# Optimization experiments

Hardware: AMD Instinct MI355X
Metric: run time of the kernel (lower is better)

Reference implementation:

```python
import jax, jax.numpy as jnp
import numpy as np

H = 32          # total heads
K = 8           # active heads per token
D = 128         # head_dim = embed_dim // active_heads
E = 1024        # embed_dim
S = 1024        # seq_len
MAX_SEQ = 8192
BASE = 10000.0
SCALE = D ** -0.5
LB_W = 0.01
ENT_W = 0.01


def _rope(v, cos, sin):
    # v: (T, D); cos/sin: (T, D)
    v1, v2 = v[:, : D // 2], v[:, D // 2:]
    rot = jnp.concatenate([-v2, v1], axis=-1)
    return v * cos + rot * sin


def setup_inputs() -> dict:
    key = jax.random.key(0)
    ks = jax.random.split(key, 6)
    x = jax.random.normal(ks[0], (1, S, E), jnp.float32)
    Wq = jax.random.normal(ks[1], (E, H * D), jnp.float32) * 0.02
    Wk = jax.random.normal(ks[2], (E, H * D), jnp.float32) * 0.02
    Wv = jax.random.normal(ks[3], (E, H * D), jnp.float32) * 0.02
    Wr = jax.random.normal(ks[4], (E, H), jnp.float32) * 0.02
    Wo = jax.random.normal(ks[5], (K * D, E), jnp.float32) * 0.02
    head_counts = jnp.zeros((1, H), jnp.int32)
    return {"x": x, "Wq": Wq, "Wk": Wk, "Wv": Wv, "Wr": Wr, "Wo": Wo,
            "head_counts": head_counts}


def reference(x, Wq, Wk, Wv, Wr, Wo, head_counts):
    # ---- routing (eval mode: no gumbel noise) ----
    logits = x @ Wr                                   # (1, S, H)
    soft_probs = jax.nn.softmax(logits, axis=-1)
    top_logits, head_idx = jax.lax.top_k(logits, K)   # (1, S, K)
    head_w = jax.nn.softmax(top_logits, axis=-1)      # (1, S, K)

    # ---- aux loss ----
    primary = head_idx[..., 0]                        # (1, S)
    one_hot_p = jax.nn.one_hot(primary, H, dtype=jnp.float32)
    f = one_hot_p.mean(axis=1)                        # (1, H)
    p = soft_probs.mean(axis=1)                       # (1, H)
    balance = H * (f * p).sum(axis=-1).mean()
    entropy = -(soft_probs * jnp.log(soft_probs + 1e-8)).sum(axis=-1)
    entropy_loss = -entropy.mean()
    z_loss = (jax.nn.logsumexp(logits, axis=-1) ** 2).mean() * 0.01
    aux_loss = LB_W * balance + ENT_W * entropy_loss + z_loss

    # ---- projections + per-token gather of selected heads ----
    q_all = (x @ Wq).reshape(1, S, H, D)
    k_all = (x @ Wk).reshape(1, S, H, D)
    v_all = (x @ Wv).reshape(1, S, H, D)
    gidx = head_idx[..., None]                        # (1, S, K, 1)
    q = jnp.take_along_axis(q_all, gidx, axis=2)[0].reshape(S * K, D)
    k = jnp.take_along_axis(k_all, gidx, axis=2)[0].reshape(S * K, D)
    v = jnp.take_along_axis(v_all, gidx, axis=2)[0].reshape(S * K, D)

    heads_flat = head_idx[0].reshape(S * K)           # (T,)

    # rank of each dispatched token within its head (exclusive prefix count)
    oh = jax.nn.one_hot(heads_flat, H, dtype=jnp.int32)   # (T, H)
    excl = jnp.cumsum(oh, axis=0) - oh
    rank = jnp.take_along_axis(excl, heads_flat[:, None], axis=1)[:, 0]
    positions = rank + head_counts[0, heads_flat]
    positions = jnp.clip(positions, 0, MAX_SEQ - 1)

    # ---- per-head RoPE with per-head position counters ----
    inv_freq = 1.0 / (BASE ** (jnp.arange(0, D, 2, dtype=jnp.float32) / D))
    freqs = positions.astype(jnp.float32)[:, None] * inv_freq[None, :]
    emb = jnp.concatenate([freqs, freqs], axis=-1)    # (T, D)
    cos, sin = jnp.cos(emb), jnp.sin(emb)
    q = _rope(q, cos, sin)
    k = _rope(k, cos, sin)

    # ---- block-diagonal-causal attention (same head, earlier dispatch order) ----
    idx = jnp.arange(S * K)
    mask = (heads_flat[:, None] == heads_flat[None, :]) & (idx[None, :] <= idx[:, None])
    scores = (q @ k.T) * SCALE                        # (T, T)
    scores = jnp.where(mask, scores, jnp.float32(-1e30))
    attn = jax.nn.softmax(scores, axis=-1)
    out = attn @ v                                    # (T, D)

    # ---- combine with routing weights + output projection ----
    out = out.reshape(S, K, D) * head_w[0][..., None]
    out = out.reshape(S, K * D) @ Wo                  # (S, E)
    output = out[None]                                # (1, S, E)

    updated_counts = head_counts + oh.sum(axis=0)[None]
    return output, updated_counts, aux_loss
```

## Files before the change

kernel.cpp:

```cpp
#include <hip/hip_runtime.h>
#include <math.h>

#define S 1024
#define E 1024
#define H 32
#define KSEL 8
#define D 128
#define HD 4096
#define SK 8192
#define MAXL 1024
#define CAP 9216
#define ATTN_SCALE 0.08838834764831845f
#define SSTR 36
#define PSTR 40

typedef _Float16 half8 __attribute__((ext_vector_type(8)));
typedef _Float16 half4 __attribute__((ext_vector_type(4)));
typedef float floatx4 __attribute__((ext_vector_type(4)));
typedef float floatx16 __attribute__((ext_vector_type(16)));
typedef float f4 __attribute__((ext_vector_type(4)));

#define GLOAD_LDS16(gsrc, ldst) \
    __builtin_amdgcn_global_load_lds( \
        (const __attribute__((address_space(1))) void*)(gsrc), \
        (__attribute__((address_space(3))) void*)(ldst), 16, 0, 0)

__global__ __launch_bounds__(256) void router_kernel(
    const float* __restrict__ x, const float* __restrict__ Wr,
    int* __restrict__ head_idx, float* __restrict__ head_w,
    float* __restrict__ pbuf, float* __restrict__ entz,
    _Float16* __restrict__ xh)
{
    int tid = threadIdx.x;
    int s = blockIdx.x * 4 + (tid >> 6);
    int lane = tid & 63;
    int h = lane & 31, half = lane >> 5;
    const float* xr = x + (size_t)s * E + half * 512;
    const float* wr = Wr + (size_t)(half * 512) * H + h;
    float acc = 0.f;
    #pragma unroll 8
    for (int e = 0; e < 512; ++e)
        acc += xr[e] * wr[e * H];
    acc += __shfl_xor(acc, 32, 64);
    float logit = acc;
    float m = logit;
    #pragma unroll
    for (int off = 16; off; off >>= 1) m = fmaxf(m, __shfl_xor(m, off, 64));
    float ex = expf(logit - m);
    float Z = ex;
    #pragma unroll
    for (int off = 16; off; off >>= 1) Z += __shfl_xor(Z, off, 64);
    float p = ex / Z;
    float es = p * logf(p + 1e-8f);
    #pragma unroll
    for (int off = 16; off; off >>= 1) es += __shfl_xor(es, off, 64);
    float lse = m + logf(Z);
    float lv = logit;
    float tv[KSEL]; int ti[KSEL];
    #pragma unroll
    for (int j = 0; j < KSEL; ++j) {
        float bv = lv; int bi = h;
        #pragma unroll
        for (int off = 16; off; off >>= 1) {
            float ov = __shfl_xor(bv, off, 64);
            int oi = __shfl_xor(bi, off, 64);
            if (ov > bv || (ov == bv && oi < bi)) { bv = ov; bi = oi; }
        }
        tv[j] = bv; ti[j] = bi;
        if (h == bi) lv = -INFINITY;
    }
    float Z2 = 0.f;
    #pragma unroll
    for (int j = 0; j < KSEL; ++j) Z2 += expf(tv[j] - tv[0]);
    if (lane < 32) pbuf[s * 32 + lane] = p;
    if (lane == 0) {
        entz[s * 2]     = es;
        entz[s * 2 + 1] = lse * lse;
        #pragma unroll
        for (int j = 0; j < KSEL; ++j) {
            head_idx[s * KSEL + j] = ti[j];
            head_w[s * KSEL + j]   = expf(tv[j] - tv[0]) / Z2;
        }
    }
    const float* xrow = x + (size_t)s * E;
    _Float16* xhrow = xh + (size_t)s * E;
    #pragma unroll
    for (int t = 0; t < 4; ++t) {
        int e = t * 256 + lane * 4;
        f4 v = *(const f4*)&xrow[e];
        half4 o;
        o.x = (_Float16)v.x; o.y = (_Float16)v.y; o.z = (_Float16)v.z; o.w = (_Float16)v.w;
        *(half4*)&xhrow[e] = o;
    }
}

__global__ __launch_bounds__(256) void aux_kernel(
    const float* __restrict__ pbuf, const float* __restrict__ entz,
    const int* __restrict__ head_idx, float* __restrict__ out_aux)
{
    int tid = threadIdx.x;
    int h = tid & 31, grp = tid >> 5;
    __shared__ float red[256], red2[256];
    __shared__ float psum[32];
    __shared__ int hist[32];
    if (tid < 32) hist[tid] = 0;
    float ps = 0.f;
    for (int s = grp; s < S; s += 8) ps += pbuf[s * 32 + h];
    red[tid] = ps;
    float es = 0.f, zs = 0.f;
    for (int s = tid; s < S; s += 256) { es += entz[s * 2]; zs += entz[s * 2 + 1]; }
    red2[tid] = es;
    __syncthreads();
    if (grp == 0) {
        float v = 0.f;
        #pragma unroll
        for (int j = 0; j < 8; ++j) v += red[j * 32 + h];
        psum[h] = v;
    }
    __syncthreads();
    red[tid] = zs;
    for (int s = tid; s < S; s += 256)
        atomicAdd(&hist[head_idx[s * KSEL]], 1);
    __syncthreads();
    for (int stp = 128; stp; stp >>= 1) {
        if (tid < stp) { red[tid] += red[tid + stp]; red2[tid] += red2[tid + stp]; }
        __syncthreads();
    }
    if (tid == 0) {
        float bal = 0.f;
        for (int hh = 0; hh < H; ++hh)
            bal += ((float)hist[hh] / (float)S) * (psum[hh] / (float)S);
        bal *= (float)H;
        float ent_loss = red2[0] / (float)S;
        float z = red[0] / (float)S * 0.01f;
        out_aux[0] = 0.01f * bal + 0.01f * ent_loss + z;
    }
}

__global__ __launch_bounds__(256) void order_kernel(
    const int* __restrict__ head_idx, const int* __restrict__ head_counts,
    int* __restrict__ order, int* __restrict__ hlen, float* __restrict__ out_counts)
{
    int h = blockIdx.x, tid = threadIdx.x;
    int wave = tid >> 6, lane = tid & 63;
    __shared__ int wtot[4];
    int base = 0;
    int hc = head_counts[h];
    int v = head_idx[tid];
    for (int c0 = 0; c0 < SK; c0 += 256) {
        int vn = (c0 + 256 < SK) ? head_idx[c0 + 256 + tid] : 0;
        bool pred = (v == h);
        unsigned long long mask = __ballot(pred);
        int within = __popcll(mask & ((1ull << lane) - 1ull));
        if (lane == 0) wtot[wave] = __popcll(mask);
        __syncthreads();
        int pre = 0, tot = 0;
        #pragma unroll
        for (int w = 0; w < 4; ++w) { int t = wtot[w]; if (w < wave) pre += t; tot += t; }
        if (pred) order[h * MAXL + base + pre + within] = c0 + tid;
        base += tot;
        __syncthreads();
        v = vn;
    }
    if (tid == 0) {
        hlen[h] = base;
        out_counts[h] = (float)(hc + base);
    }
}

__global__ void offs_kernel(const int* __restrict__ hlen, int* __restrict__ hstart)
{
    if (threadIdx.x == 0 && blockIdx.x == 0) {
        int acc = 0;
        for (int h = 0; h < H; ++h) {
            hstart[h] = acc;
            acc += (hlen[h] + 31) & ~31;
        }
    }
}

__global__ __launch_bounds__(256) void convW_kernel(
    const float* __restrict__ Wq, const float* __restrict__ Wk,
    const float* __restrict__ Wv, const float* __restrict__ Wo,
    _Float16* __restrict__ Wqkt, _Float16* __restrict__ Wot)
{
    int z = blockIdx.z;
    if (z == 3 && blockIdx.y >= 16) return;
    const float* W = (z == 0) ? Wq : (z == 1) ? Wk : (z == 2) ? Wv : Wo;
    _Float16* T = (z < 3) ? (Wqkt + (size_t)z * HD * E) : Wot;
    int C = (z < 3) ? HD : 1024;
    int r0 = blockIdx.x * 64, c0 = blockIdx.y * 64;
    int t = threadIdx.x;
    __shared__ float tile[64][65];
    #pragma unroll
    for (int p = 0; p < 4; ++p) {
        int idx = p * 256 + t;
        int r = idx >> 4, cq = (idx & 15) * 4;
        f4 v = *(const f4*)&W[(size_t)(r0 + r) * C + c0 + cq];
        tile[r][cq] = v.x; tile[r][cq + 1] = v.y; tile[r][cq + 2] = v.z; tile[r][cq + 3] = v.w;
    }
    __syncthreads();
    #pragma unroll
    for (int p = 0; p < 4; ++p) {
        int idx = p * 256 + t;
        int c = idx >> 4, rq = (idx & 15) * 4;
        half4 o;
        o.x = (_Float16)tile[rq][c];
        o.y = (_Float16)tile[rq + 1][c];
        o.z = (_Float16)tile[rq + 2][c];
        o.w = (_Float16)tile[rq + 3][c];
        *(half4*)&T[(size_t)(c0 + c) * 1024 + r0 + rq] = o;
    }
}

__global__ __launch_bounds__(256) void qkv_mfma(
    const _Float16* __restrict__ xh, const _Float16* __restrict__ Wt,
    const int* __restrict__ order, const int* __restrict__ hlen,
    const int* __restrict__ hstart, const int* __restrict__ head_counts,
    _Float16* __restrict__ qh, _Float16* __restrict__ kh, _Float16* __restrict__ vT)
{
    int xid = blockIdx.x;
    int qkv = xid >> 5, h = xid & 31;
    int rt = blockIdx.y;
    int len = hlen[h];
    int row0 = rt * 64;
    if (row0 >= len) return;
    int hb = hstart[h];
    int lenp = (len + 31) & ~31;
    int tid = threadIdx.x, wave = tid >> 6, lane = tid & 63;
    int wm = wave >> 1, wn = wave & 1;
    int l32 = lane & 31, g = lane >> 5;

    __shared__ _Float16 As[2][64 * 64];
    __shared__ _Float16 Bs[2][128 * 64];
    __shared__ int stok[64];

    if (tid < 64) {
        int r = row0 + tid;
        stok[tid] = (r < len) ? (order[h * MAXL + r] >> 3) : 0;
    }
    __syncthreads();

    const _Float16* Wb = Wt + (size_t)((qkv * H + h) * D) * E;

    auto stage = [&](int buf, int k0) {
        #pragma unroll
        for (int it = 0; it < 2; ++it) {
            int f = it * 256 + tid;
            int row = f >> 3, c = f & 7;
            int sc = c ^ (row & 7);
            const _Float16* src = xh + (size_t)stok[row] * E + k0 + sc * 8;
            GLOAD_LDS16(src, &As[buf][f * 8]);
        }
        #pragma unroll
        for (int it = 0; it < 4; ++it) {
            int f = it * 256 + tid;
            int row = f >> 3, c = f & 7;
            int sc = c ^ (row & 7);
            const _Float16* src = Wb + (size_t)row * E + k0 + sc * 8;
            GLOAD_LDS16(src, &Bs[buf][f * 8]);
        }
    };

    floatx16 acc[2] = {};
    int arow = wm * 32 + l32;

    auto compute = [&](int buf) {
        #pragma unroll
        for (int ks = 0; ks < 4; ++ks) {
            int wchunk = ks * 2 + g;
            half8 af = *(const half8*)&As[buf][arow * 64 + (wchunk ^ (arow & 7)) * 8];
            #pragma unroll
            for (int nf = 0; nf < 2; ++nf) {
                int brow = wn * 64 + nf * 32 + l32;
                half8 bf = *(const half8*)&Bs[buf][brow * 64 + (wchunk ^ (brow & 7)) * 8];
                acc[nf] = __builtin_amdgcn_mfma_f32_32x32x16_f16(af, bf, acc[nf], 0, 0, 0);
            }
        }
    };

    stage(0, 0);
    __syncthreads();
    int buf = 0;
    for (int k0 = 64; k0 < E; k0 += 64) {
        stage(buf ^ 1, k0);
        compute(buf);
        __syncthreads();
        buf ^= 1;
    }
    compute(buf);

    if (qkv < 2) {
        _Float16* dst = (qkv == 0) ? qh : kh;
        float* scr = (float*)&Bs[0][0];
        __syncthreads();
        #pragma unroll
        for (int nf = 0; nf < 2; ++nf) {
            int col = wn * 64 + nf * 32 + l32;
            #pragma unroll
            for (int reg = 0; reg < 16; ++reg) {
                int rl = wm * 32 + (reg & 3) + 8 * (reg >> 2) + 4 * g;
                scr[rl * 128 + col] = acc[nf][reg];
            }
        }
        __syncthreads();
        int hc = head_counts[h];
        #pragma unroll
        for (int pass = 0; pass < 16; ++pass) {
            int idx = pass * 256 + tid;
            int r = idx >> 6, d2 = idx & 63;
            int slot = row0 + r;
            if (slot < len) {
                float v1 = scr[r * 128 + d2], v2 = scr[r * 128 + 64 + d2];
                int p = slot + hc;
                p = p < 0 ? 0 : (p > 8191 ? 8191 : p);
                float inv = exp2f((float)d2 * -0.20762050f);
                float ang = (float)p * inv;
                float cs = cosf(ang), sn = sinf(ang);
                _Float16* dp = dst + ((size_t)hb + slot) * D;
                dp[d2]      = (_Float16)(v1 * cs - v2 * sn);
                dp[d2 + 64] = (_Float16)(v2 * cs + v1 * sn);
            }
        }
    } else {
        #pragma unroll
        for (int nf = 0; nf < 2; ++nf) {
            int col = wn * 64 + nf * 32 + l32;
            #pragma unroll
            for (int q4 = 0; q4 < 4; ++q4) {
                int slot0 = row0 + wm * 32 + 8 * q4 + 4 * g;
                _Float16* vp = vT + (size_t)hb * D + (size_t)col * lenp + slot0;
                if (slot0 + 3 < len) {
                    half4 o;
                    o.x = (_Float16)acc[nf][q4 * 4 + 0];
                    o.y = (_Float16)acc[nf][q4 * 4 + 1];
                    o.z = (_Float16)acc[nf][q4 * 4 + 2];
                    o.w = (_Float16)acc[nf][q4 * 4 + 3];
                    *(half4*)vp = o;
                } else {
                    #pragma unroll
                    for (int r2 = 0; r2 < 4; ++r2)
                        if (slot0 + r2 < len) vp[r2] = (_Float16)acc[nf][q4 * 4 + r2];
                }
            }
        }
    }
}

__global__ __launch_bounds__(64) void attn_mfma(
    const _Float16* __restrict__ qh, const _Float16* __restrict__ kh,
    const _Float16* __restrict__ vT,
    const int* __restrict__ order, const int* __restrict__ hlen,
    const int* __restrict__ hstart, const float* __restrict__ head_w,
    _Float16* __restrict__ ao)
{
    int h = blockIdx.x >> 5, qt = blockIdx.x & 31;
    int len = hlen[h];
    int row0 = qt * 32;
    if (row0 >= len) return;
    int hb = hstart[h];
    int lenp = (len + 31) & ~31;
    int lane = threadIdx.x;
    int l32 = lane & 31, g = lane >> 5;
    int srow = lane >> 1, shalf = lane & 1;

    __shared__ float Sld[32 * SSTR];
    __shared__ _Float16 Pld[32 * PSTR];
    __shared__ float alphaLd[32];
    __shared__ float scLd[32];
    __shared__ int flatLd[32];

    if (lane < 32) {
        int r = row0 + lane;
        flatLd[lane] = (r < len) ? order[h * MAXL + r] : -1;
    }

    const _Float16* qrow = qh + ((size_t)hb + row0 + l32) * D;
    half8 qf[8];
    #pragma unroll
    for (int t = 0; t < 8; ++t) qf[t] = *(const half8*)(qrow + t * 16 + g * 8);

    floatx16 O[4] = {};
    float m_run = -INFINITY, l_run = 0.f;
    __syncthreads();

    half8 kf[8], kfn[8], vv[8];
    {
        const _Float16* krow = kh + ((size_t)hb + l32) * D;
        #pragma unroll
        for (int t = 0; t < 8; ++t) kf[t] = *(const half8*)(krow + t * 16 + g * 8);
    }

    for (int kt = 0; kt <= qt; ++kt) {
        int col0 = kt * 32;
        floatx16 Sc = {};
        #pragma unroll
        for (int t = 0; t < 8; ++t)
            Sc = __builtin_amdgcn_mfma_f32_32x32x16_f16(qf[t], kf[t], Sc, 0, 0, 0);
        #pragma unroll
        for (int nt = 0; nt < 4; ++nt) {
            const _Float16* vp = vT + (size_t)hb * D + (size_t)(nt * 32 + l32) * lenp + col0;
            vv[nt * 2]     = *(const half8*)(vp + g * 8);
            vv[nt * 2 + 1] = *(const half8*)(vp + 16 + g * 8);
        }
        if (kt < qt) {
            const _Float16* krow = kh + ((size_t)hb + col0 + 32 + l32) * D;
            #pragma unroll
            for (int t = 0; t < 8; ++t) kfn[t] = *(const half8*)(krow + t * 16 + g * 8);
        }
        bool diag = (kt == qt);
        #pragma unroll
        for (int reg = 0; reg < 16; ++reg) {
            int row = (reg & 3) + 8 * (reg >> 2) + 4 * g;
            float s = Sc[reg] * ATTN_SCALE;
            if (diag && l32 > row) s = -1e30f;
            Sld[row * SSTR + l32] = s;
        }
        __syncthreads();
        const float* sp = &Sld[srow * SSTR + shalf * 16];
        float va[16];
        *(f4*)(va)      = *(const f4*)(sp);
        *(f4*)(va + 4)  = *(const f4*)(sp + 4);
        *(f4*)(va + 8)  = *(const f4*)(sp + 8);
        *(f4*)(va + 12) = *(const f4*)(sp + 12);
        float mt_ = va[0];
        #pragma unroll
        for (int j = 1; j < 16; ++j) mt_ = fmaxf(mt_, va[j]);
        mt_ = fmaxf(mt_, __shfl_xor(mt_, 1, 64));
        float m_new = fmaxf(m_run, mt_);
        float alpha = __expf(m_run - m_new);
        float p[16], tsum = 0.f;
        #pragma unroll
        for (int j = 0; j < 16; ++j) { p[j] = __expf(va[j] - m_new); tsum += p[j]; }
        tsum += __shfl_xor(tsum, 1, 64);
        l_run = l_run * alpha + tsum;
        m_run = m_new;
        half8 ph0, ph1;
        #pragma unroll
        for (int j = 0; j < 8; ++j) { ph0[j] = (_Float16)p[j]; ph1[j] = (_Float16)p[j + 8]; }
        *(half8*)&Pld[srow * PSTR + shalf * 16]     = ph0;
        *(half8*)&Pld[srow * PSTR + shalf * 16 + 8] = ph1;
        if (shalf == 0) alphaLd[srow] = alpha;
        __syncthreads();
        f4 al[4];
        #pragma unroll
        for (int qq = 0; qq < 4; ++qq) al[qq] = *(const f4*)&alphaLd[4 * g + 8 * qq];
        #pragma unroll
        for (int reg = 0; reg < 16; ++reg) {
            float av = al[reg >> 2][reg & 3];
            O[0][reg] *= av; O[1][reg] *= av; O[2][reg] *= av; O[3][reg] *= av;
        }
        half8 pf0 = *(const half8*)&Pld[l32 * PSTR + g * 8];
        half8 pf1 = *(const half8*)&Pld[l32 * PSTR + 16 + g * 8];
        #pragma unroll
        for (int nt = 0; nt < 4; ++nt) {
            O[nt] = __builtin_amdgcn_mfma_f32_32x32x16_f16(pf0, vv[nt * 2],     O[nt], 0, 0, 0);
            O[nt] = __builtin_amdgcn_mfma_f32_32x32x16_f16(pf1, vv[nt * 2 + 1], O[nt], 0, 0, 0);
        }
        __syncthreads();
        #pragma unroll
        for (int t = 0; t < 8; ++t) kf[t] = kfn[t];
    }
    if (shalf == 0) {
        int flat = flatLd[srow];
        float hw = (flat >= 0) ? head_w[flat] : 0.f;
        scLd[srow] = hw / l_run;
    }
    __syncthreads();
    float scr[16]; int flr[16];
    #pragma unroll
    for (int reg = 0; reg < 16; ++reg) {
        int row = (reg & 3) + 8 * (reg >> 2) + 4 * g;
        scr[reg] = scLd[row];
        flr[reg] = flatLd[row];
    }
    #pragma unroll
    for (int nt = 0; nt < 4; ++nt) {
        int col = nt * 32 + l32;
        #pragma unroll
        for (int reg = 0; reg < 16; ++reg) {
            if (flr[reg] >= 0)
                ao[(size_t)flr[reg] * D + col] = (_Float16)(O[nt][reg] * scr[reg]);
        }
    }
}

__global__ __launch_bounds__(256) void out_mfma(
    const _Float16* __restrict__ A, const _Float16* __restrict__ Bt,
    float* __restrict__ C)
{
    int n0 = blockIdx.x * 64, m0 = blockIdx.y * 64;
    int tid = threadIdx.x, wave = tid >> 6, lane = tid & 63;
    int wm = wave >> 1, wn = wave & 1;
    int l32 = lane & 31, g = lane >> 5;

    __shared__ _Float16 As[2][64 * 64];
    __shared__ _Float16 Bs[2][64 * 64];

    auto stage = [&](int buf, int k0) {
        #pragma unroll
        for (int it = 0; it < 2; ++it) {
            int f = it * 256 + tid;
            int row = f >> 3, c = f & 7;
            int sc = c ^ (row & 7);
            GLOAD_LDS16(A + (size_t)(m0 + row) * 1024 + k0 + sc * 8, &As[buf][f * 8]);
        }
        #pragma unroll
        for (int it = 0; it < 2; ++it) {
            int f = it * 256 + tid;
            int row = f >> 3, c = f & 7;
            int sc = c ^ (row & 7);
            GLOAD_LDS16(Bt + (size_t)(n0 + row) * 1024 + k0 + sc * 8, &Bs[buf][f * 8]);
        }
    };

    floatx16 acc = {};
    int arow = wm * 32 + l32;
    int brow = wn * 32 + l32;

    auto compute = [&](int buf) {
        #pragma unroll
        for (int ks = 0; ks < 4; ++ks) {
            int wchunk = ks * 2 + g;
            half8 af = *(const half8*)&As[buf][arow * 64 + (wchunk ^ (arow & 7)) * 8];
            half8 bf = *(const half8*)&Bs[buf][brow * 64 + (wchunk ^ (brow & 7)) * 8];
            acc = __builtin_amdgcn_mfma_f32_32x32x16_f16(af, bf, acc, 0, 0, 0);
        }
    };

    stage(0, 0);
    __syncthreads();
    int buf = 0;
    for (int k0 = 64; k0 < 1024; k0 += 64) {
        stage(buf ^ 1, k0);
        compute(buf);
        __syncthreads();
        buf ^= 1;
    }
    compute(buf);

    int col = n0 + wn * 32 + l32;
    #pragma unroll
    for (int reg = 0; reg < 16; ++reg) {
        int row = m0 + wm * 32 + (reg & 3) + 8 * (reg >> 2) + 4 * g;
        C[(size_t)row * 1024 + col] = acc[reg];
    }
}

extern "C" void kernel_launch(void* const* d_in, const int* in_sizes, int n_in,
                              void* d_out, int out_size, void* d_ws, size_t ws_size,
                              hipStream_t stream)
{
    const float* x  = (const float*)d_in[0];
    const float* Wq = (const float*)d_in[1];
    const float* Wk = (const float*)d_in[2];
    const float* Wv = (const float*)d_in[3];
    const float* Wr = (const float*)d_in[4];
    const float* Wo = (const float*)d_in[5];
    const int* head_counts = (const int*)d_in[6];
    float* out = (float*)d_out;

    float* head_w = (float*)d_ws;
    float* pbuf   = head_w + SK;
    float* entz   = pbuf + S * 32;
    int* head_idx = (int*)(entz + S * 2);
    int* order    = head_idx + SK;
    int* hlen     = order + H * MAXL;
    int* hstart   = hlen + 32;
    _Float16* xh   = (_Float16*)(hstart + 32);
    _Float16* aoh  = xh + (size_t)S * E;
    _Float16* Wqkt = aoh + (size_t)SK * D;
    _Float16* Wot  = Wqkt + (size_t)3 * HD * E;
    _Float16* qh   = Wot + (size_t)1024 * 1024;
    _Float16* kh   = qh + (size_t)CAP * D;
    _Float16* vT   = kh + (size_t)CAP * D;

    convW_kernel<<<dim3(16, 64, 4), 256, 0, stream>>>(Wq, Wk, Wv, Wo, Wqkt, Wot);
    router_kernel<<<S / 4, 256, 0, stream>>>(x, Wr, head_idx, head_w, pbuf, entz, xh);
    order_kernel<<<H, 256, 0, stream>>>(head_idx, head_counts, order, hlen,
                                        out + (size_t)S * E);
    offs_kernel<<<1, 64, 0, stream>>>(hlen, hstart);
    qkv_mfma<<<dim3(96, 16), 256, 0, stream>>>(xh, Wqkt, order, hlen, hstart, head_counts,
                                               qh, kh, vT);
    attn_mfma<<<H * 32, 64, 0, stream>>>(qh, kh, vT, order, hlen, hstart, head_w, aoh);
    out_mfma<<<dim3(16, 16), 256, 0, stream>>>(aoh, Wot, out);
    aux_kernel<<<1, 256, 0, stream>>>(pbuf, entz, head_idx, out + (size_t)S * E + H);
}
```

Before: 239.2 us.

## Split attention KV loop across two waves, fold aux and offsets kernels away

Attention blocks now use two waves that each handle alternating key tiles, then merge their partial softmax states (max and sum) through shared memory before the scaled output is written. This shortens the serial per-block loop for long causal rows. The aux-loss kernel is merged into order_kernel as an extra block, and the offset kernel is replaced by recomputing the per-head prefix sum inside qkv and attention. The router dot product also uses four accumulators. Together these remove two launches and add shared-memory use and a merge step in attention.

```diff
diff --git a/kernel.cpp b/kernel.cpp
--- a/kernel.cpp
+++ b/kernel.cpp
@@ -37,10 +37,15 @@
     int h = lane & 31, half = lane >> 5;
     const float* xr = x + (size_t)s * E + half * 512;
     const float* wr = Wr + (size_t)(half * 512) * H + h;
-    float acc = 0.f;
-    #pragma unroll 8
-    for (int e = 0; e < 512; ++e)
-        acc += xr[e] * wr[e * H];
+    float a0 = 0.f, a1 = 0.f, a2 = 0.f, a3 = 0.f;
+    #pragma unroll 4
+    for (int e = 0; e < 512; e += 4) {
+        a0 += xr[e]     * wr[e * H];
+        a1 += xr[e + 1] * wr[(e + 1) * H];
+        a2 += xr[e + 2] * wr[(e + 2) * H];
+        a3 += xr[e + 3] * wr[(e + 3) * H];
+    }
+    float acc = (a0 + a1) + (a2 + a3);
     acc += __shfl_xor(acc, 32, 64);
     float logit = acc;
     float m = logit;
@@ -94,54 +99,52 @@
     }
 }
 
-__global__ __launch_bounds__(256) void aux_kernel(
-    const float* __restrict__ pbuf, const float* __restrict__ entz,
-    const int* __restrict__ head_idx, float* __restrict__ out_aux)
-{
-    int tid = threadIdx.x;
-    int h = tid & 31, grp = tid >> 5;
-    __shared__ float red[256], red2[256];
-    __shared__ float psum[32];
-    __shared__ int hist[32];
-    if (tid < 32) hist[tid] = 0;
-    float ps = 0.f;
-    for (int s = grp; s < S; s += 8) ps += pbuf[s * 32 + h];
-    red[tid] = ps;
-    float es = 0.f, zs = 0.f;
-    for (int s = tid; s < S; s += 256) { es += entz[s * 2]; zs += entz[s * 2 + 1]; }
-    red2[tid] = es;
-    __syncthreads();
-    if (grp == 0) {
-        float v = 0.f;
-        #pragma unroll
-        for (int j = 0; j < 8; ++j) v += red[j * 32 + h];
-        psum[h] = v;
-    }
-    __syncthreads();
-    red[tid] = zs;
-    for (int s = tid; s < S; s += 256)
-        atomicAdd(&hist[head_idx[s * KSEL]], 1);
-    __syncthreads();
-    for (int stp = 128; stp; stp >>= 1) {
-        if (tid < stp) { red[tid] += red[tid + stp]; red2[tid] += red2[tid + stp]; }
-        __syncthreads();
-    }
-    if (tid == 0) {
-        float bal = 0.f;
-        for (int hh = 0; hh < H; ++hh)
-            bal += ((float)hist[hh] / (float)S) * (psum[hh] / (float)S);
-        bal *= (float)H;
-        float ent_loss = red2[0] / (float)S;
-        float z = red[0] / (float)S * 0.01f;
-        out_aux[0] = 0.01f * bal + 0.01f * ent_loss + z;
-    }
-}
-
 __global__ __launch_bounds__(256) void order_kernel(
     const int* __restrict__ head_idx, const int* __restrict__ head_counts,
-    int* __restrict__ order, int* __restrict__ hlen, float* __restrict__ out_counts)
+    int* __restrict__ order, int* __restrict__ hlen, float* __restrict__ out_counts,
+    const float* __restrict__ pbuf, const float* __restrict__ entz,
+    float* __restrict__ out_aux)
 {
     int h = blockIdx.x, tid = threadIdx.x;
+    if (h == H) {
+        int hh = tid & 31, grp = tid >> 5;
+        __shared__ float red[256], red2[256];
+        __shared__ float psum[32];
+        __shared__ int hist[32];
+        if (tid < 32) hist[tid] = 0;
+        float ps = 0.f;
+        for (int s = grp; s < S; s += 8) ps += pbuf[s * 32 + hh];
+        red[tid] = ps;
+        float es = 0.f, zs = 0.f;
+        for (int s = tid; s < S; s += 256) { es += entz[s * 2]; zs += entz[s * 2 + 1]; }
+        red2[tid] = es;
+        __syncthreads();
+        if (grp == 0) {
+            float v = 0.f;
+            #pragma unroll
+            for (int j = 0; j < 8; ++j) v += red[j * 32 + hh];
+            psum[hh] = v;
+        }
+        __syncthreads();
+        red[tid] = zs;
+        for (int s = tid; s < S; s += 256)
+            atomicAdd(&hist[head_idx[s * KSEL]], 1);
+        __syncthreads();
+        for (int stp = 128; stp; stp >>= 1) {
+            if (tid < stp) { red[tid] += red[tid + stp]; red2[tid] += red2[tid + stp]; }
+            __syncthreads();
+        }
+        if (tid == 0) {
+            float bal = 0.f;
+            for (int j = 0; j < H; ++j)
+                bal += ((float)hist[j] / (float)S) * (psum[j] / (float)S);
+            bal *= (float)H;
+            float ent_loss = red2[0] / (float)S;
+            float z = red[0] / (float)S * 0.01f;
+            out_aux[0] = 0.01f * bal + 0.01f * ent_loss + z;
+        }
+        return;
+    }
     int wave = tid >> 6, lane = tid & 63;
     __shared__ int wtot[4];
     int base = 0;
@@ -165,17 +168,6 @@
     if (tid == 0) {
         hlen[h] = base;
         out_counts[h] = (float)(hc + base);
-    }
-}
-
-__global__ void offs_kernel(const int* __restrict__ hlen, int* __restrict__ hstart)
-{
-    if (threadIdx.x == 0 && blockIdx.x == 0) {
-        int acc = 0;
-        for (int h = 0; h < H; ++h) {
-            hstart[h] = acc;
-            acc += (hlen[h] + 31) & ~31;
-        }
     }
 }
 
@@ -216,7 +208,7 @@
 __global__ __launch_bounds__(256) void qkv_mfma(
     const _Float16* __restrict__ xh, const _Float16* __restrict__ Wt,
     const int* __restrict__ order, const int* __restrict__ hlen,
-    const int* __restrict__ hstart, const int* __restrict__ head_counts,
+    const int* __restrict__ head_counts,
     _Float16* __restrict__ qh, _Float16* __restrict__ kh, _Float16* __restrict__ vT)
 {
     int xid = blockIdx.x;
@@ -225,7 +217,8 @@
     int len = hlen[h];
     int row0 = rt * 64;
     if (row0 >= len) return;
-    int hb = hstart[h];
+    int hb = 0;
+    for (int i = 0; i < h; ++i) hb += (hlen[i] + 31) & ~31;
     int lenp = (len + 31) & ~31;
     int tid = threadIdx.x, wave = tid >> 6, lane = tid & 63;
     int wm = wave >> 1, wn = wave & 1;
@@ -347,32 +340,35 @@
     }
 }
 
-__global__ __launch_bounds__(64) void attn_mfma(
+__global__ __launch_bounds__(128) void attn_mfma(
     const _Float16* __restrict__ qh, const _Float16* __restrict__ kh,
     const _Float16* __restrict__ vT,
     const int* __restrict__ order, const int* __restrict__ hlen,
-    const int* __restrict__ hstart, const float* __restrict__ head_w,
-    _Float16* __restrict__ ao)
+    const float* __restrict__ head_w, _Float16* __restrict__ ao)
 {
     int h = blockIdx.x >> 5, qt = blockIdx.x & 31;
     int len = hlen[h];
     int row0 = qt * 32;
     if (row0 >= len) return;
-    int hb = hstart[h];
+    int hb = 0;
+    for (int i = 0; i < h; ++i) hb += (hlen[i] + 31) & ~31;
     int lenp = (len + 31) & ~31;
-    int lane = threadIdx.x;
+    int tid = threadIdx.x;
+    int w = tid >> 6, lane = tid & 63;
     int l32 = lane & 31, g = lane >> 5;
     int srow = lane >> 1, shalf = lane & 1;
 
-    __shared__ float Sld[32 * SSTR];
-    __shared__ _Float16 Pld[32 * PSTR];
-    __shared__ float alphaLd[32];
-    __shared__ float scLd[32];
+    __shared__ float Sld[2][32 * SSTR];
+    __shared__ _Float16 Pld[2][32 * PSTR];
+    __shared__ float alphaLd[2][32];
+    __shared__ float mlLd[32][4];
+    __shared__ float facLd[32][3];
     __shared__ int flatLd[32];
-
-    if (lane < 32) {
-        int r = row0 + lane;
-        flatLd[lane] = (r < len) ? order[h * MAXL + r] : -1;
+    __shared__ float Obuf[32][128];
+
+    if (tid < 32) {
+        int r = row0 + tid;
+        flatLd[tid] = (r < len) ? order[h * MAXL + r] : -1;
     }
 
     const _Float16* qrow = qh + ((size_t)hb + row0 + l32) * D;
@@ -382,105 +378,125 @@
 
     floatx16 O[4] = {};
     float m_run = -INFINITY, l_run = 0.f;
+
+    if (w <= qt) {
+        half8 kf[8], kfn[8], vv[8];
+        {
+            const _Float16* krow = kh + ((size_t)hb + w * 32 + l32) * D;
+            #pragma unroll
+            for (int t = 0; t < 8; ++t) kf[t] = *(const half8*)(krow + t * 16 + g * 8);
+        }
+        for (int kt = w; kt <= qt; kt += 2) {
+            int col0 = kt * 32;
+            floatx16 Sc = {};
+            #pragma unroll
+            for (int t = 0; t < 8; ++t)
+                Sc = __builtin_amdgcn_mfma_f32_32x32x16_f16(qf[t], kf[t], Sc, 0, 0, 0);
+            #pragma unroll
+            for (int nt = 0; nt < 4; ++nt) {
+                const _Float16* vp = vT + (size_t)hb * D + (size_t)(nt * 32 + l32) * lenp + col0;
+                vv[nt * 2]     = *(const half8*)(vp + g * 8);
+                vv[nt * 2 + 1] = *(const half8*)(vp + 16 + g * 8);
+            }
+            if (kt + 2 <= qt) {
+                const _Float16* krow = kh + ((size_t)hb + col0 + 64 + l32) * D;
+                #pragma unroll
+                for (int t = 0; t < 8; ++t) kfn[t] = *(const half8*)(krow + t * 16 + g * 8);
+            }
+            bool diag = (kt == qt);
+            #pragma unroll
+            for (int reg = 0; reg < 16; ++reg) {
+                int row = (reg & 3) + 8 * (reg >> 2) + 4 * g;
+                float s = Sc[reg] * ATTN_SCALE;
+                if (diag && l32 > row) s = -1e30f;
+                Sld[w][row * SSTR + l32] = s;
+            }
+            __builtin_amdgcn_wave_barrier();
+            const float* sp = &Sld[w][srow * SSTR + shalf * 16];
+            float va[16];
+            *(f4*)(va)      = *(const f4*)(sp);
+            *(f4*)(va + 4)  = *(const f4*)(sp + 4);
+            *(f4*)(va + 8)  = *(const f4*)(sp + 8);
+            *(f4*)(va + 12) = *(const f4*)(sp + 12);
+            float mt_ = va[0];
+            #pragma unroll
+            for (int j = 1; j < 16; ++j) mt_ = fmaxf(mt_, va[j]);
+            mt_ = fmaxf(mt_, __shfl_xor(mt_, 1, 64));
+            float m_new = fmaxf(m_run, mt_);
+            float alpha = __expf(m_run - m_new);
+            float p[16], tsum = 0.f;
+            #pragma unroll
+            for (int j = 0; j < 16; ++j) { p[j] = __expf(va[j] - m_new); tsum += p[j]; }
+            tsum += __shfl_xor(tsum, 1, 64);
+            l_run = l_run * alpha + tsum;
+            m_run = m_new;
+            half8 ph0, ph1;
+            #pragma unroll
+            for (int j = 0; j < 8; ++j) { ph0[j] = (_Float16)p[j]; ph1[j] = (_Float16)p[j + 8]; }
+            *(half8*)&Pld[w][srow * PSTR + shalf * 16]     = ph0;
+            *(half8*)&Pld[w][srow * PSTR + shalf * 16 + 8] = ph1;
+            if (shalf == 0) alphaLd[w][srow] = alpha;
+            __builtin_amdgcn_wave_barrier();
+            f4 al[4];
+            #pragma unroll
+            for (int qq = 0; qq < 4; ++qq) al[qq] = *(const f4*)&alphaLd[w][4 * g + 8 * qq];
+            #pragma unroll
+            for (int reg = 0; reg < 16; ++reg) {
+                float av = al[reg >> 2][reg & 3];
+                O[0][reg] *= av; O[1][reg] *= av; O[2][reg] *= av; O[3][reg] *= av;
+            }
+            half8 pf0 = *(const half8*)&Pld[w][l32 * PSTR + g * 8];
+            half8 pf1 = *(const half8*)&Pld[w][l32 * PSTR + 16 + g * 8];
+            #pragma unroll
+            for (int nt = 0; nt < 4; ++nt) {
+                O[nt] = __builtin_amdgcn_mfma_f32_32x32x16_f16(pf0, vv[nt * 2],     O[nt], 0, 0, 0);
+                O[nt] = __builtin_amdgcn_mfma_f32_32x32x16_f16(pf1, vv[nt * 2 + 1], O[nt], 0, 0, 0);
+            }
+            __builtin_amdgcn_wave_barrier();
+            #pragma unroll
+            for (int t = 0; t < 8; ++t) kf[t] = kfn[t];
+        }
+    }
+    if (shalf == 0) { mlLd[srow][w * 2] = m_run; mlLd[srow][w * 2 + 1] = l_run; }
     __syncthreads();
-
-    half8 kf[8], kfn[8], vv[8];
-    {
-        const _Float16* krow = kh + ((size_t)hb + l32) * D;
-        #pragma unroll
-        for (int t = 0; t < 8; ++t) kf[t] = *(const half8*)(krow + t * 16 + g * 8);
-    }
-
-    for (int kt = 0; kt <= qt; ++kt) {
-        int col0 = kt * 32;
-        floatx16 Sc = {};
-        #pragma unroll
-        for (int t = 0; t < 8; ++t)
-            Sc = __builtin_amdgcn_mfma_f32_32x32x16_f16(qf[t], kf[t], Sc, 0, 0, 0);
+    if (tid < 32) {
+        float m0 = mlLd[tid][0], l0 = mlLd[tid][1];
+        float m1 = mlLd[tid][2], l1 = mlLd[tid][3];
+        float ms = fmaxf(m0, m1);
+        float f0 = __expf(m0 - ms), f1 = __expf(m1 - ms);
+        float lt = f0 * l0 + f1 * l1;
+        int flat = flatLd[tid];
+        float hw = (flat >= 0) ? head_w[flat] : 0.f;
+        facLd[tid][0] = f1;
+        facLd[tid][1] = hw / lt;
+        facLd[tid][2] = f0;
+    }
+    __syncthreads();
+    if (w == 1) {
         #pragma unroll
         for (int nt = 0; nt < 4; ++nt) {
-            const _Float16* vp = vT + (size_t)hb * D + (size_t)(nt * 32 + l32) * lenp + col0;
-            vv[nt * 2]     = *(const half8*)(vp + g * 8);
-            vv[nt * 2 + 1] = *(const half8*)(vp + 16 + g * 8);
-        }
-        if (kt < qt) {
-            const _Float16* krow = kh + ((size_t)hb + col0 + 32 + l32) * D;
-            #pragma unroll
-            for (int t = 0; t < 8; ++t) kfn[t] = *(const half8*)(krow + t * 16 + g * 8);
-        }
-        bool diag = (kt == qt);
-        #pragma unroll
-        for (int reg = 0; reg < 16; ++reg) {
-            int row = (reg & 3) + 8 * (reg >> 2) + 4 * g;
-            float s = Sc[reg] * ATTN_SCALE;
-            if (diag && l32 > row) s = -1e30f;
-            Sld[row * SSTR + l32] = s;
-        }
-        __syncthreads();
-        const float* sp = &Sld[srow * SSTR + shalf * 16];
-        float va[16];
-        *(f4*)(va)      = *(const f4*)(sp);
-        *(f4*)(va + 4)  = *(const f4*)(sp + 4);
-        *(f4*)(va + 8)  = *(const f4*)(sp + 8);
-        *(f4*)(va + 12) = *(const f4*)(sp + 12);
-        float mt_ = va[0];
-        #pragma unroll
-        for (int j = 1; j < 16; ++j) mt_ = fmaxf(mt_, va[j]);
-        mt_ = fmaxf(mt_, __shfl_xor(mt_, 1, 64));
-        float m_new = fmaxf(m_run, mt_);
-        float alpha = __expf(m_run - m_new);
-        float p[16], tsum = 0.f;
-        #pragma unroll
-        for (int j = 0; j < 16; ++j) { p[j] = __expf(va[j] - m_new); tsum += p[j]; }
-        tsum += __shfl_xor(tsum, 1, 64);
-        l_run = l_run * alpha + tsum;
-        m_run = m_new;
-        half8 ph0, ph1;
-        #pragma unroll
-        for (int j = 0; j < 8; ++j) { ph0[j] = (_Float16)p[j]; ph1[j] = (_Float16)p[j + 8]; }
-        *(half8*)&Pld[srow * PSTR + shalf * 16]     = ph0;
-        *(half8*)&Pld[srow * PSTR + shalf * 16 + 8] = ph1;
-        if (shalf == 0) alphaLd[srow] = alpha;
-        __syncthreads();
-        f4 al[4];
-        #pragma unroll
-        for (int qq = 0; qq < 4; ++qq) al[qq] = *(const f4*)&alphaLd[4 * g + 8 * qq];
-        #pragma unroll
-        for (int reg = 0; reg < 16; ++reg) {
-            float av = al[reg >> 2][reg & 3];
-            O[0][reg] *= av; O[1][reg] *= av; O[2][reg] *= av; O[3][reg] *= av;
-        }
-        half8 pf0 = *(const half8*)&Pld[l32 * PSTR + g * 8];
-        half8 pf1 = *(const half8*)&Pld[l32 * PSTR + 16 + g * 8];
+            int col = nt * 32 + l32;
+            #pragma unroll
+            for (int reg = 0; reg < 16; ++reg) {
+                int row = (reg & 3) + 8 * (reg >> 2) + 4 * g;
+                Obuf[row][col] = O[nt][reg] * facLd[row][0];
+            }
+        }
+    }
+    __syncthreads();
+    if (w == 0) {
         #pragma unroll
         for (int nt = 0; nt < 4; ++nt) {
-            O[nt] = __builtin_amdgcn_mfma_f32_32x32x16_f16(pf0, vv[nt * 2],     O[nt], 0, 0, 0);
-            O[nt] = __builtin_amdgcn_mfma_f32_32x32x16_f16(pf1, vv[nt * 2 + 1], O[nt], 0, 0, 0);
-        }
-        __syncthreads();
-        #pragma unroll
-        for (int t = 0; t < 8; ++t) kf[t] = kfn[t];
-    }
-    if (shalf == 0) {
-        int flat = flatLd[srow];
-        float hw = (flat >= 0) ? head_w[flat] : 0.f;
-        scLd[srow] = hw / l_run;
-    }
-    __syncthreads();
-    float scr[16]; int flr[16];
-    #pragma unroll
-    for (int reg = 0; reg < 16; ++reg) {
-        int row = (reg & 3) + 8 * (reg >> 2) + 4 * g;
-        scr[reg] = scLd[row];
-        flr[reg] = flatLd[row];
-    }
-    #pragma unroll
-    for (int nt = 0; nt < 4; ++nt) {
-        int col = nt * 32 + l32;
-        #pragma unroll
-        for (int reg = 0; reg < 16; ++reg) {
-            if (flr[reg] >= 0)
-                ao[(size_t)flr[reg] * D + col] = (_Float16)(O[nt][reg] * scr[reg]);
+            int col = nt * 32 + l32;
+            #pragma unroll
+            for (int reg = 0; reg < 16; ++reg) {
+                int row = (reg & 3) + 8 * (reg >> 2) + 4 * g;
+                int flat = flatLd[row];
+                if (flat >= 0) {
+                    float val = (O[nt][reg] * facLd[row][2] + Obuf[row][col]) * facLd[row][1];
+                    ao[(size_t)flat * D + col] = (_Float16)val;
+                }
+            }
         }
     }
 }
@@ -566,8 +582,7 @@
     int* head_idx = (int*)(entz + S * 2);
     int* order    = head_idx + SK;
     int* hlen     = order + H * MAXL;
-    int* hstart   = hlen + 32;
-    _Float16* xh   = (_Float16*)(hstart + 32);
+    _Float16* xh   = (_Float16*)(hlen + 64);
     _Float16* aoh  = xh + (size_t)S * E;
     _Float16* Wqkt = aoh + (size_t)SK * D;
     _Float16* Wot  = Wqkt + (size_t)3 * HD * E;
@@ -577,12 +592,11 @@
 
     convW_kernel<<<dim3(16, 64, 4), 256, 0, stream>>>(Wq, Wk, Wv, Wo, Wqkt, Wot);
     router_kernel<<<S / 4, 256, 0, stream>>>(x, Wr, head_idx, head_w, pbuf, entz, xh);
-    order_kernel<<<H, 256, 0, stream>>>(head_idx, head_counts, order, hlen,
-                                        out + (size_t)S * E);
-    offs_kernel<<<1, 64, 0, stream>>>(hlen, hstart);
-    qkv_mfma<<<dim3(96, 16), 256, 0, stream>>>(xh, Wqkt, order, hlen, hstart, head_counts,
+    order_kernel<<<H + 1, 256, 0, stream>>>(head_idx, head_counts, order, hlen,
+                                            out + (size_t)S * E, pbuf, entz,
+                                            out + (size_t)S * E + H);
+    qkv_mfma<<<dim3(96, 16), 256, 0, stream>>>(xh, Wqkt, order, hlen, head_counts,
                                                qh, kh, vT);
-    attn_mfma<<<H * 32, 64, 0, stream>>>(qh, kh, vT, order, hlen, hstart, head_w, aoh);
+    attn_mfma<<<H * 32, 128, 0, stream>>>(qh, kh, vT, order, hlen, head_w, aoh);
     out_mfma<<<dim3(16, 16), 256, 0, stream>>>(aoh, Wot, out);
-    aux_kernel<<<1, 256, 0, stream>>>(pbuf, entz, head_idx, out + (size_t)S * E + H);
 }
```

Result: faster. 226.2 us (-5.4%).
